# Kernel optimization log

Hardware: AMD Instinct MI355X
Metric: run time of the kernel (lower is better)

Reference implementation:

```python
import jax, jax.numpy as jnp
import numpy as np

DT = 1.0  # forward arg dt, fixed to its default
NOISE_KEY = 42

def _lin_init(k, fan_in, fan_out):
    kw, kb = jax.random.split(k)
    s = 1.0 / np.sqrt(fan_in)
    W = jax.random.uniform(kw, (fan_in, fan_out), minval=-s, maxval=s, dtype=jnp.float32)
    b = jax.random.uniform(kb, (fan_out,), minval=-s, maxval=s, dtype=jnp.float32)
    return W, b

def setup_inputs() -> dict:
    key = jax.random.key(0)
    ks = jax.random.split(key, 10)
    batch, d_model, hidden = 8, 512, 64
    in_dim = d_model + 2  # ctx + y + t
    W_f1, b_f1 = _lin_init(ks[0], in_dim, hidden)
    W_f2, b_f2 = _lin_init(ks[1], hidden, hidden)
    W_f3, b_f3 = _lin_init(ks[2], hidden, 1)
    W_g1, b_g1 = _lin_init(ks[3], in_dim, hidden)
    W_g2, b_g2 = _lin_init(ks[4], hidden, 1)
    W_mu, b_mu = _lin_init(ks[5], d_model, 1)
    W_sig, b_sig = _lin_init(ks[6], d_model, 1)
    h_t = jax.random.normal(ks[7], (batch, d_model), dtype=jnp.float32)
    # positive prices (log is taken); uniform in [0.5, 2.0)
    initial_price = jax.random.uniform(ks[8], (batch,), minval=0.5, maxval=2.0, dtype=jnp.float32)
    return dict(h_t=h_t, initial_price=initial_price,
                W_f1=W_f1, b_f1=b_f1, W_f2=W_f2, b_f2=b_f2, W_f3=W_f3, b_f3=b_f3,
                W_g1=W_g1, b_g1=b_g1, W_g2=W_g2, b_g2=b_g2,
                W_mu=W_mu, b_mu=b_mu, W_sig=W_sig, b_sig=b_sig,
                horizon=128, n_paths=4096)

def reference(h_t, initial_price, W_f1, b_f1, W_f2, b_f2, W_f3, b_f3,
              W_g1, b_g1, W_g2, b_g2, W_mu, b_mu, W_sig, b_sig,
              horizon, n_paths):
    batch, d = h_t.shape
    dtype = h_t.dtype
    mu = (h_t @ W_mu + b_mu)[:, 0]
    sigma = jax.nn.softplus(h_t @ W_sig + b_sig)[:, 0] + 1e-6
    # flatten (batch, n_paths) -> BN rows, broadcast context per path
    ctx = jnp.broadcast_to(h_t[:, None, :], (batch, n_paths, d)).reshape(batch * n_paths, d)
    y0 = jnp.broadcast_to(jnp.log(initial_price)[:, None], (batch, n_paths)).reshape(-1, 1)
    keys = jax.random.split(jax.random.key(NOISE_KEY), horizon)
    ts = jnp.arange(horizon, dtype=dtype) * jnp.asarray(DT, dtype)
    sqrt_dt = jnp.sqrt(jnp.asarray(DT, dtype))
    def step(y, xs):
        t, k = xs
        t_vec = jnp.broadcast_to(t, (y.shape[0], 1)).astype(dtype)
        inp = jnp.concatenate([ctx, y, t_vec], axis=-1)  # (BN, d+2)
        h1 = jax.nn.silu(inp @ W_f1 + b_f1)
        h2 = jax.nn.silu(h1 @ W_f2 + b_f2)
        f = h2 @ W_f3 + b_f3                              # drift (BN,1)
        g = jax.nn.softplus(jax.nn.silu(inp @ W_g1 + b_g1) @ W_g2 + b_g2) + 1e-6
        dW = jax.random.normal(k, y.shape, dtype) * sqrt_dt
        y_new = y + f * jnp.asarray(DT, dtype) + g * dW   # Euler-Maruyama (ito, diagonal)
        return y_new, y_new[:, 0]
    _, ys = jax.lax.scan(step, y0, (ts, keys))            # (horizon, BN)
    log_paths = jnp.clip(ys.T, -20.0, 20.0)               # (BN, horizon)
    paths = jnp.exp(log_paths).reshape(batch, n_paths, horizon)
    return paths, mu, sigma
```

## Files before the change

kernel.cpp:

```cpp
#include <hip/hip_runtime.h>
#include <stdint.h>

#define HOR 128
#define NPATH 4096
#define BATCH 8
#define DM 512
#define H 64
#define BN (BATCH*NPATH)

typedef __attribute__((ext_vector_type(8))) short s16x8;
typedef __attribute__((ext_vector_type(4))) float f32x4;

__device__ __forceinline__ uint32_t rotl32(uint32_t x, int r) {
  return (x << r) | (x >> (32 - r));
}

__device__ __forceinline__ void tf2x32(uint32_t k0, uint32_t k1,
                                       uint32_t& x0, uint32_t& x1) {
  uint32_t k2 = k0 ^ k1 ^ 0x1BD11BDAu;
  x0 += k0; x1 += k1;
#define TFR4(a,b,c,d) \
  x0 += x1; x1 = rotl32(x1,a); x1 ^= x0; \
  x0 += x1; x1 = rotl32(x1,b); x1 ^= x0; \
  x0 += x1; x1 = rotl32(x1,c); x1 ^= x0; \
  x0 += x1; x1 = rotl32(x1,d); x1 ^= x0;
  TFR4(13,15,26,6)  x0 += k1; x1 += k2 + 1u;
  TFR4(17,29,16,24) x0 += k2; x1 += k0 + 2u;
  TFR4(13,15,26,6)  x0 += k0; x1 += k1 + 3u;
  TFR4(17,29,16,24) x0 += k1; x1 += k2 + 4u;
  TFR4(13,15,26,6)  x0 += k2; x1 += k0 + 5u;
#undef TFR4
}

__device__ __forceinline__ float rcpf(float x) { return __builtin_amdgcn_rcpf(x); }
__device__ __forceinline__ float siluf(float x) {
  return x * rcpf(1.0f + __expf(-x));
}
__device__ __forceinline__ float softplusf(float x) {
  return fmaxf(x, 0.0f) + log1pf(__expf(-fabsf(x)));
}

__device__ __forceinline__ float bits_to_normal(uint32_t bits) {
  uint32_t fb = (bits >> 9) | 0x3F800000u;
  float f = __uint_as_float(fb) - 1.0f;
  float u = fmaf(f, 2.0f, -0.99999994f);
  u = fmaxf(u, -0.99999994f);
  float w = -log1pf(-u * u);
  float p;
  if (w < 5.0f) {
    w = w - 2.5f;
    p = 2.81022636e-08f;
    p = fmaf(p, w, 3.43273939e-07f);
    p = fmaf(p, w, -3.5233877e-06f);
    p = fmaf(p, w, -4.39150654e-06f);
    p = fmaf(p, w, 0.00021858087f);
    p = fmaf(p, w, -0.00125372503f);
    p = fmaf(p, w, -0.00417768164f);
    p = fmaf(p, w, 0.246640727f);
    p = fmaf(p, w, 1.50140941f);
  } else {
    w = sqrtf(w) - 3.0f;
    p = -0.000200214257f;
    p = fmaf(p, w, 0.000100950558f);
    p = fmaf(p, w, 0.00134934322f);
    p = fmaf(p, w, -0.00367342844f);
    p = fmaf(p, w, 0.00573950773f);
    p = fmaf(p, w, -0.0076224613f);
    p = fmaf(p, w, 0.00943887047f);
    p = fmaf(p, w, 1.00167406f);
    p = fmaf(p, w, 2.83297682f);
  }
  return 1.41421356237f * (p * u);
}

__device__ __forceinline__ uint32_t pack_hi16(uint32_t hi_src, uint32_t lo_src) {
  return __builtin_amdgcn_perm(hi_src, lo_src, 0x07060302u);
}

union FragU { uint32_t u[4]; s16x8 v; };

__device__ __forceinline__ void split3(const float (&x)[8],
                                       s16x8& fh, s16x8& fm, s16x8& fl) {
  FragU Hh, Mm, Ll;
  #pragma unroll
  for (int d = 0; d < 4; ++d) {
    float x0 = x[2*d], x1 = x[2*d+1];
    uint32_t a0 = __float_as_uint(x0), a1 = __float_as_uint(x1);
    float r10 = x0 - __uint_as_float(a0 & 0xFFFF0000u);
    float r11 = x1 - __uint_as_float(a1 & 0xFFFF0000u);
    uint32_t m0 = __float_as_uint(r10), m1 = __float_as_uint(r11);
    float r20 = r10 - __uint_as_float(m0 & 0xFFFF0000u);
    float r21 = r11 - __uint_as_float(m1 & 0xFFFF0000u);
    Hh.u[d] = pack_hi16(a1, a0);
    Mm.u[d] = pack_hi16(m1, m0);
    Ll.u[d] = pack_hi16(__float_as_uint(r21), __float_as_uint(r20));
  }
  fh = Hh.v; fm = Mm.v; fl = Ll.v;
}

#define MFMA16(A, B, C) __builtin_amdgcn_mfma_f32_16x16x32_bf16((A), (B), (C), 0, 0, 0)


__global__ void k_pre(const float* __restrict__ h_t,
                      const float* __restrict__ W_f1, const float* __restrict__ b_f1,
                      const float* __restrict__ W_g1, const float* __restrict__ b_g1,
                      const float* __restrict__ W_mu, const float* __restrict__ b_mu,
                      const float* __restrict__ W_sig, const float* __restrict__ b_sig,
                      float* __restrict__ out, float* __restrict__ ws) {
  int j = threadIdx.x;
  int b = blockIdx.x;
  if (b == 8) {
    uint32_t* keyA = (uint32_t*)ws + 1024;
    uint32_t* keyB = (uint32_t*)ws + 1152;
    for (int t = j; t < HOR; t += 64) {
      uint32_t x0 = 0u, x1 = (uint32_t)t;
      tf2x32(0u, 42u, x0, x1);
      keyA[t] = x0; keyB[t] = x1;
    }
    return;
  }
  const float* h = h_t + b * DM;
  float accF = b_f1[j], accG = b_g1[j];
  float pm = 0.0f, ps = 0.0f;
  #pragma unroll 4
  for (int d = 0; d < DM; ++d) {
    float hv = h[d];
    accF = fmaf(hv, W_f1[d * H + j], accF);
    accG = fmaf(hv, W_g1[d * H + j], accG);
  }
  ws[b * H + j] = accF;
  ws[512 + b * H + j] = accG;
  for (int d = j; d < DM; d += 64) {
    pm = fmaf(h[d], W_mu[d], pm);
    ps = fmaf(h[d], W_sig[d], ps);
  }
  #pragma unroll
  for (int off = 32; off > 0; off >>= 1) {
    pm += __shfl_down(pm, off);
    ps += __shfl_down(ps, off);
  }
  if (j == 0) {
    out[BN * HOR + b] = pm + b_mu[0];
    out[BN * HOR + 8 + b] = softplusf(ps + b_sig[0]) + 1e-6f;
  }
}

__global__ __launch_bounds__(256, 2)
void k_sde(const float* __restrict__ ip,
           const float* __restrict__ W_f1, const float* __restrict__ W_f2,
           const float* __restrict__ b_f2, const float* __restrict__ W_f3,
           const float* __restrict__ b_f3, const float* __restrict__ W_g1,
           const float* __restrict__ W_g2, const float* __restrict__ b_g2,
           float* __restrict__ out, const float* __restrict__ ws) {
  __shared__ __align__(16) float sW2[H * H];
  __shared__ __align__(16) float sF1y[H], sF1t[H], sBF[H];
  __shared__ __align__(16) float sGy[H], sGt[H], sBG[H], sG2[H];
  __shared__ __align__(16) float sF3[H], sBf2[H];
  __shared__ uint32_t sKA[HOR], sKB[HOR];

  const int tid  = threadIdx.x;
  const int rblk = blockIdx.x * 64;
  const int b    = rblk >> 12;

  #pragma unroll
  for (int m = 0; m < 16; ++m) sW2[tid + 256 * m] = W_f2[tid + 256 * m];
  if (tid < 64) {
    sF1y[tid] = W_f1[512 * H + tid];
    sF1t[tid] = W_f1[513 * H + tid];
    sGy[tid]  = W_g1[512 * H + tid];
    sGt[tid]  = W_g1[513 * H + tid];
    sF3[tid]  = W_f3[tid];
    sG2[tid]  = W_g2[tid];
    sBf2[tid] = b_f2[tid];
  } else if (tid < 128) {
    int i = tid - 64;
    sBF[i] = ws[b * H + i];
    sBG[i] = ws[512 + b * H + i];
  } else {
    const uint32_t* kws = (const uint32_t*)ws;
    int t = tid - 128;
    sKA[t] = kws[1024 + t];
    sKB[t] = kws[1152 + t];
  }
  __syncthreads();

  const int l  = tid & 63;
  const int wv = tid >> 6;
  const int rl = l & 15;
  const int h  = l >> 4;
  const int r  = rblk + wv * 16 + rl;

  s16x8 aw[4][2][3];
  #pragma unroll
  for (int mt = 0; mt < 4; ++mt) {
    #pragma unroll
    for (int s = 0; s < 2; ++s) {
      float xv[8];
      #pragma unroll
      for (int e = 0; e < 8; ++e)
        xv[e] = sW2[(32 * s + 8 * h + e) * H + 16 * mt + rl];
      split3(xv, aw[mt][s][0], aw[mt][s][1], aw[mt][s][2]);
    }
  }

  f32x4 f3v[4], bf2v[4];
  #pragma unroll
  for (int mt = 0; mt < 4; ++mt) {
    f3v[mt]  = *(const f32x4*)&sF3[16 * mt + 4 * h];
    bf2v[mt] = *(const f32x4*)&sBf2[16 * mt + 4 * h];
  }

  f32x4 wy[2][2], wt1[2][2], wb[2][2];
  #pragma unroll
  for (int s = 0; s < 2; ++s) {
    const int k0 = 32 * s + 8 * h;
    wy[s][0]  = *(const f32x4*)&sF1y[k0]; wy[s][1]  = *(const f32x4*)&sF1y[k0 + 4];
    wt1[s][0] = *(const f32x4*)&sF1t[k0]; wt1[s][1] = *(const f32x4*)&sF1t[k0 + 4];
    wb[s][0]  = *(const f32x4*)&sBF[k0];  wb[s][1]  = *(const f32x4*)&sBF[k0 + 4];
  }

  const float bf3 = b_f3[0];
  const float bg2 = b_g2[0];
  float y  = logf(ip[b]);
  float zz = 0.0f;
  float sb0 = 0.f, sb1 = 0.f, sb2 = 0.f, sb3 = 0.f;

  #pragma unroll 1
  for (int t = 0; t < HOR; ++t) {
    if ((t & 3) == 0) {
      const int tk = t + h;
      uint32_t x0 = 0u, x1 = (uint32_t)r;
      tf2x32(sKA[tk], sKB[tk], x0, x1);
      zz = bits_to_normal(x0 ^ x1);
    }
    const float z  = __shfl(zz, rl + 16 * (t & 3));
    const float tt = (float)t;

    f32x4 c[4];
    #pragma unroll
    for (int mt = 0; mt < 4; ++mt) c[mt] = bf2v[mt];

    s16x8 bh[2], bm[2], bl[2];
    #pragma unroll
    for (int s = 0; s < 2; ++s) {
      float hv[8];
      #pragma unroll
      for (int d2 = 0; d2 < 2; ++d2) {
        const f32x4 a_ = wy[s][d2], b_ = wt1[s][d2], cc = wb[s][d2];
        hv[4*d2+0] = siluf(fmaf(y, a_.x, fmaf(tt, b_.x, cc.x)));
        hv[4*d2+1] = siluf(fmaf(y, a_.y, fmaf(tt, b_.y, cc.y)));
        hv[4*d2+2] = siluf(fmaf(y, a_.z, fmaf(tt, b_.z, cc.z)));
        hv[4*d2+3] = siluf(fmaf(y, a_.w, fmaf(tt, b_.w, cc.w)));
      }
      split3(hv, bh[s], bm[s], bl[s]);
    }

    #pragma unroll
    for (int s = 0; s < 2; ++s) {
      #pragma unroll
      for (int mt = 0; mt < 4; ++mt) c[mt] = MFMA16(aw[mt][s][0], bh[s], c[mt]);
      #pragma unroll
      for (int mt = 0; mt < 4; ++mt) c[mt] = MFMA16(aw[mt][s][0], bm[s], c[mt]);
      #pragma unroll
      for (int mt = 0; mt < 4; ++mt) c[mt] = MFMA16(aw[mt][s][1], bh[s], c[mt]);
      #pragma unroll
      for (int mt = 0; mt < 4; ++mt) c[mt] = MFMA16(aw[mt][s][1], bm[s], c[mt]);
      #pragma unroll
      for (int mt = 0; mt < 4; ++mt) c[mt] = MFMA16(aw[mt][s][0], bl[s], c[mt]);
      #pragma unroll
      for (int mt = 0; mt < 4; ++mt) c[mt] = MFMA16(aw[mt][s][2], bh[s], c[mt]);
    }

    int kg = 8 * h;
    asm volatile("" : "+v"(kg));
    float ga = 0.0f;
    #pragma unroll
    for (int s = 0; s < 2; ++s) {
      const int k0 = kg + 32 * s;
      const f32x4 gy0 = *(const f32x4*)&sGy[k0], gy1 = *(const f32x4*)&sGy[k0 + 4];
      const f32x4 gt0 = *(const f32x4*)&sGt[k0], gt1 = *(const f32x4*)&sGt[k0 + 4];
      const f32x4 gb0 = *(const f32x4*)&sBG[k0], gb1 = *(const f32x4*)&sBG[k0 + 4];
      const f32x4 g20 = *(const f32x4*)&sG2[k0], g21 = *(const f32x4*)&sG2[k0 + 4];
      ga = fmaf(siluf(fmaf(y, gy0.x, fmaf(tt, gt0.x, gb0.x))), g20.x, ga);
      ga = fmaf(siluf(fmaf(y, gy0.y, fmaf(tt, gt0.y, gb0.y))), g20.y, ga);
      ga = fmaf(siluf(fmaf(y, gy0.z, fmaf(tt, gt0.z, gb0.z))), g20.z, ga);
      ga = fmaf(siluf(fmaf(y, gy0.w, fmaf(tt, gt0.w, gb0.w))), g20.w, ga);
      ga = fmaf(siluf(fmaf(y, gy1.x, fmaf(tt, gt1.x, gb1.x))), g21.x, ga);
      ga = fmaf(siluf(fmaf(y, gy1.y, fmaf(tt, gt1.y, gb1.y))), g21.y, ga);
      ga = fmaf(siluf(fmaf(y, gy1.z, fmaf(tt, gt1.z, gb1.z))), g21.z, ga);
      ga = fmaf(siluf(fmaf(y, gy1.w, fmaf(tt, gt1.w, gb1.w))), g21.w, ga);
    }
    ga += __shfl_xor(ga, 16);
    ga += __shfl_xor(ga, 32);
    const float gg = softplusf(bg2 + ga) + 1e-6f;

    float fa = 0.0f;
    #pragma unroll
    for (int mt = 0; mt < 4; ++mt) {
      fa = fmaf(siluf(c[mt].x), f3v[mt].x, fa);
      fa = fmaf(siluf(c[mt].y), f3v[mt].y, fa);
      fa = fmaf(siluf(c[mt].z), f3v[mt].z, fa);
      fa = fmaf(siluf(c[mt].w), f3v[mt].w, fa);
    }
    fa += __shfl_xor(fa, 16);
    fa += __shfl_xor(fa, 32);

    y = (y + (bf3 + fa)) + gg * z;
    const float yl = fminf(fmaxf(y, -20.0f), 20.0f);
    const float e  = __expf(yl);
    if (((t >> 2) & 3) == h) { sb0 = sb1; sb1 = sb2; sb2 = sb3; sb3 = e; }
    if ((t & 15) == 15) {
      f32x4 v; v.x = sb0; v.y = sb1; v.z = sb2; v.w = sb3;
      *(f32x4*)&out[(size_t)r * HOR + (t & ~15) + 4 * h] = v;
    }
  }
}

extern "C" void kernel_launch(void* const* d_in, const int* in_sizes, int n_in,
                              void* d_out, int out_size, void* d_ws, size_t ws_size,
                              hipStream_t stream) {
  const float* h_t   = (const float*)d_in[0];
  const float* ip    = (const float*)d_in[1];
  const float* W_f1  = (const float*)d_in[2];
  const float* b_f1  = (const float*)d_in[3];
  const float* W_f2  = (const float*)d_in[4];
  const float* b_f2  = (const float*)d_in[5];
  const float* W_f3  = (const float*)d_in[6];
  const float* b_f3  = (const float*)d_in[7];
  const float* W_g1  = (const float*)d_in[8];
  const float* b_g1  = (const float*)d_in[9];
  const float* W_g2  = (const float*)d_in[10];
  const float* b_g2  = (const float*)d_in[11];
  const float* W_mu  = (const float*)d_in[12];
  const float* b_mu  = (const float*)d_in[13];
  const float* W_sig = (const float*)d_in[14];
  const float* b_sig = (const float*)d_in[15];
  float* out = (float*)d_out;
  float* ws  = (float*)d_ws;

  hipLaunchKernelGGL(k_pre, dim3(9), dim3(64), 0, stream,
                     h_t, W_f1, b_f1, W_g1, b_g1, W_mu, b_mu, W_sig, b_sig, out, ws);
  hipLaunchKernelGGL(k_sde, dim3(BN / 64), dim3(256), 0, stream,
                     ip, W_f1, W_f2, b_f2, W_f3, b_f3, W_g1, W_g2, b_g2, out, ws);
}
```

Before: 528.9 us.

## Process two path groups per wave and pair SiLU reciprocals

Each wave now advances two independent 16-row groups of paths at once, so the serial recurrence gets two interleaved dependency chains. The MFMA weight fragments are reused across both groups and the block count is halved. SiLU is computed in pairs that share one reciprocal, softplus uses a fast log, and the reductions use split partial sums with a three-way shuffle. The cost is higher register pressure (launch bounds relaxed to 1 block), fewer blocks overall, and slightly different rounding.

```diff
diff --git a/kernel.cpp b/kernel.cpp
--- a/kernel.cpp
+++ b/kernel.cpp
@@ -36,8 +36,18 @@
 __device__ __forceinline__ float siluf(float x) {
   return x * rcpf(1.0f + __expf(-x));
 }
+__device__ __forceinline__ void silu2(float x0, float x1, float& o0, float& o1) {
+  const float e0 = __expf(-x0), e1 = __expf(-x1);
+  const float d0 = 1.0f + e0,   d1 = 1.0f + e1;
+  const float r  = rcpf(d0 * d1);
+  o0 = x0 * (r * d1);
+  o1 = x1 * (r * d0);
+}
 __device__ __forceinline__ float softplusf(float x) {
   return fmaxf(x, 0.0f) + log1pf(__expf(-fabsf(x)));
+}
+__device__ __forceinline__ float softplus_fast(float x) {
+  return fmaxf(x, 0.0f) + __logf(1.0f + __expf(-fabsf(x)));
 }
 
 __device__ __forceinline__ float bits_to_normal(uint32_t bits) {
@@ -145,7 +155,7 @@
   }
 }
 
-__global__ __launch_bounds__(256, 2)
+__global__ __launch_bounds__(256, 1)
 void k_sde(const float* __restrict__ ip,
            const float* __restrict__ W_f1, const float* __restrict__ W_f2,
            const float* __restrict__ b_f2, const float* __restrict__ W_f3,
@@ -159,7 +169,7 @@
   __shared__ uint32_t sKA[HOR], sKB[HOR];
 
   const int tid  = threadIdx.x;
-  const int rblk = blockIdx.x * 64;
+  const int rblk = blockIdx.x * 128;
   const int b    = rblk >> 12;
 
   #pragma unroll
@@ -188,7 +198,8 @@
   const int wv = tid >> 6;
   const int rl = l & 15;
   const int h  = l >> 4;
-  const int r  = rblk + wv * 16 + rl;
+  const int rA = rblk + wv * 32 + rl;
+  const int rB = rA + 16;
 
   s16x8 aw[4][2][3];
   #pragma unroll
@@ -221,97 +232,189 @@
 
   const float bf3 = b_f3[0];
   const float bg2 = b_g2[0];
-  float y  = logf(ip[b]);
-  float zz = 0.0f;
-  float sb0 = 0.f, sb1 = 0.f, sb2 = 0.f, sb3 = 0.f;
+  float yA = logf(ip[b]);
+  float yB = yA;
+  float zzA = 0.0f, zzB = 0.0f;
+  float sbA0 = 0.f, sbA1 = 0.f, sbA2 = 0.f, sbA3 = 0.f;
+  float sbB0 = 0.f, sbB1 = 0.f, sbB2 = 0.f, sbB3 = 0.f;
 
   #pragma unroll 1
   for (int t = 0; t < HOR; ++t) {
     if ((t & 3) == 0) {
       const int tk = t + h;
-      uint32_t x0 = 0u, x1 = (uint32_t)r;
+      uint32_t x0 = 0u, x1 = (uint32_t)rA;
       tf2x32(sKA[tk], sKB[tk], x0, x1);
-      zz = bits_to_normal(x0 ^ x1);
-    }
-    const float z  = __shfl(zz, rl + 16 * (t & 3));
+      zzA = bits_to_normal(x0 ^ x1);
+      uint32_t y0 = 0u, y1 = (uint32_t)rB;
+      tf2x32(sKA[tk], sKB[tk], y0, y1);
+      zzB = bits_to_normal(y0 ^ y1);
+    }
+    const float zA = __shfl(zzA, rl + 16 * (t & 3));
+    const float zB = __shfl(zzB, rl + 16 * (t & 3));
     const float tt = (float)t;
 
-    f32x4 c[4];
+    f32x4 cA[4], cB[4];
     #pragma unroll
-    for (int mt = 0; mt < 4; ++mt) c[mt] = bf2v[mt];
-
-    s16x8 bh[2], bm[2], bl[2];
+    for (int mt = 0; mt < 4; ++mt) { cA[mt] = bf2v[mt]; cB[mt] = bf2v[mt]; }
+
+    s16x8 bhA[2], bmA[2], blA[2], bhB[2], bmB[2], blB[2];
     #pragma unroll
     for (int s = 0; s < 2; ++s) {
-      float hv[8];
+      float pvA[8], pvB[8], hvA[8], hvB[8];
       #pragma unroll
       for (int d2 = 0; d2 < 2; ++d2) {
         const f32x4 a_ = wy[s][d2], b_ = wt1[s][d2], cc = wb[s][d2];
-        hv[4*d2+0] = siluf(fmaf(y, a_.x, fmaf(tt, b_.x, cc.x)));
-        hv[4*d2+1] = siluf(fmaf(y, a_.y, fmaf(tt, b_.y, cc.y)));
-        hv[4*d2+2] = siluf(fmaf(y, a_.z, fmaf(tt, b_.z, cc.z)));
-        hv[4*d2+3] = siluf(fmaf(y, a_.w, fmaf(tt, b_.w, cc.w)));
+        const float tb0 = fmaf(tt, b_.x, cc.x);
+        const float tb1 = fmaf(tt, b_.y, cc.y);
+        const float tb2 = fmaf(tt, b_.z, cc.z);
+        const float tb3 = fmaf(tt, b_.w, cc.w);
+        pvA[4*d2+0] = fmaf(yA, a_.x, tb0);  pvB[4*d2+0] = fmaf(yB, a_.x, tb0);
+        pvA[4*d2+1] = fmaf(yA, a_.y, tb1);  pvB[4*d2+1] = fmaf(yB, a_.y, tb1);
+        pvA[4*d2+2] = fmaf(yA, a_.z, tb2);  pvB[4*d2+2] = fmaf(yB, a_.z, tb2);
+        pvA[4*d2+3] = fmaf(yA, a_.w, tb3);  pvB[4*d2+3] = fmaf(yB, a_.w, tb3);
       }
-      split3(hv, bh[s], bm[s], bl[s]);
+      silu2(pvA[0], pvA[1], hvA[0], hvA[1]); silu2(pvB[0], pvB[1], hvB[0], hvB[1]);
+      silu2(pvA[2], pvA[3], hvA[2], hvA[3]); silu2(pvB[2], pvB[3], hvB[2], hvB[3]);
+      silu2(pvA[4], pvA[5], hvA[4], hvA[5]); silu2(pvB[4], pvB[5], hvB[4], hvB[5]);
+      silu2(pvA[6], pvA[7], hvA[6], hvA[7]); silu2(pvB[6], pvB[7], hvB[6], hvB[7]);
+      split3(hvA, bhA[s], bmA[s], blA[s]);
+      split3(hvB, bhB[s], bmB[s], blB[s]);
     }
 
     #pragma unroll
     for (int s = 0; s < 2; ++s) {
       #pragma unroll
-      for (int mt = 0; mt < 4; ++mt) c[mt] = MFMA16(aw[mt][s][0], bh[s], c[mt]);
-      #pragma unroll
-      for (int mt = 0; mt < 4; ++mt) c[mt] = MFMA16(aw[mt][s][0], bm[s], c[mt]);
-      #pragma unroll
-      for (int mt = 0; mt < 4; ++mt) c[mt] = MFMA16(aw[mt][s][1], bh[s], c[mt]);
-      #pragma unroll
-      for (int mt = 0; mt < 4; ++mt) c[mt] = MFMA16(aw[mt][s][1], bm[s], c[mt]);
-      #pragma unroll
-      for (int mt = 0; mt < 4; ++mt) c[mt] = MFMA16(aw[mt][s][0], bl[s], c[mt]);
-      #pragma unroll
-      for (int mt = 0; mt < 4; ++mt) c[mt] = MFMA16(aw[mt][s][2], bh[s], c[mt]);
+      for (int mt = 0; mt < 4; ++mt) { cA[mt] = MFMA16(aw[mt][s][0], bhA[s], cA[mt]);
+                                       cB[mt] = MFMA16(aw[mt][s][0], bhB[s], cB[mt]); }
+      #pragma unroll
+      for (int mt = 0; mt < 4; ++mt) { cA[mt] = MFMA16(aw[mt][s][0], bmA[s], cA[mt]);
+                                       cB[mt] = MFMA16(aw[mt][s][0], bmB[s], cB[mt]); }
+      #pragma unroll
+      for (int mt = 0; mt < 4; ++mt) { cA[mt] = MFMA16(aw[mt][s][1], bhA[s], cA[mt]);
+                                       cB[mt] = MFMA16(aw[mt][s][1], bhB[s], cB[mt]); }
+      #pragma unroll
+      for (int mt = 0; mt < 4; ++mt) { cA[mt] = MFMA16(aw[mt][s][1], bmA[s], cA[mt]);
+                                       cB[mt] = MFMA16(aw[mt][s][1], bmB[s], cB[mt]); }
+      #pragma unroll
+      for (int mt = 0; mt < 4; ++mt) { cA[mt] = MFMA16(aw[mt][s][0], blA[s], cA[mt]);
+                                       cB[mt] = MFMA16(aw[mt][s][0], blB[s], cB[mt]); }
+      #pragma unroll
+      for (int mt = 0; mt < 4; ++mt) { cA[mt] = MFMA16(aw[mt][s][2], bhA[s], cA[mt]);
+                                       cB[mt] = MFMA16(aw[mt][s][2], bhB[s], cB[mt]); }
     }
 
     int kg = 8 * h;
     asm volatile("" : "+v"(kg));
-    float ga = 0.0f;
-    #pragma unroll
-    for (int s = 0; s < 2; ++s) {
-      const int k0 = kg + 32 * s;
+    float gA0, gA1, gA2, gA3, gB0, gB1, gB2, gB3;
+    {
+      const int k0 = kg;
       const f32x4 gy0 = *(const f32x4*)&sGy[k0], gy1 = *(const f32x4*)&sGy[k0 + 4];
       const f32x4 gt0 = *(const f32x4*)&sGt[k0], gt1 = *(const f32x4*)&sGt[k0 + 4];
       const f32x4 gb0 = *(const f32x4*)&sBG[k0], gb1 = *(const f32x4*)&sBG[k0 + 4];
       const f32x4 g20 = *(const f32x4*)&sG2[k0], g21 = *(const f32x4*)&sG2[k0 + 4];
-      ga = fmaf(siluf(fmaf(y, gy0.x, fmaf(tt, gt0.x, gb0.x))), g20.x, ga);
-      ga = fmaf(siluf(fmaf(y, gy0.y, fmaf(tt, gt0.y, gb0.y))), g20.y, ga);
-      ga = fmaf(siluf(fmaf(y, gy0.z, fmaf(tt, gt0.z, gb0.z))), g20.z, ga);
-      ga = fmaf(siluf(fmaf(y, gy0.w, fmaf(tt, gt0.w, gb0.w))), g20.w, ga);
-      ga = fmaf(siluf(fmaf(y, gy1.x, fmaf(tt, gt1.x, gb1.x))), g21.x, ga);
-      ga = fmaf(siluf(fmaf(y, gy1.y, fmaf(tt, gt1.y, gb1.y))), g21.y, ga);
-      ga = fmaf(siluf(fmaf(y, gy1.z, fmaf(tt, gt1.z, gb1.z))), g21.z, ga);
-      ga = fmaf(siluf(fmaf(y, gy1.w, fmaf(tt, gt1.w, gb1.w))), g21.w, ga);
-    }
-    ga += __shfl_xor(ga, 16);
-    ga += __shfl_xor(ga, 32);
-    const float gg = softplusf(bg2 + ga) + 1e-6f;
-
-    float fa = 0.0f;
-    #pragma unroll
-    for (int mt = 0; mt < 4; ++mt) {
-      fa = fmaf(siluf(c[mt].x), f3v[mt].x, fa);
-      fa = fmaf(siluf(c[mt].y), f3v[mt].y, fa);
-      fa = fmaf(siluf(c[mt].z), f3v[mt].z, fa);
-      fa = fmaf(siluf(c[mt].w), f3v[mt].w, fa);
-    }
-    fa += __shfl_xor(fa, 16);
-    fa += __shfl_xor(fa, 32);
-
-    y = (y + (bf3 + fa)) + gg * z;
-    const float yl = fminf(fmaxf(y, -20.0f), 20.0f);
-    const float e  = __expf(yl);
-    if (((t >> 2) & 3) == h) { sb0 = sb1; sb1 = sb2; sb2 = sb3; sb3 = e; }
+      const float t0 = fmaf(tt, gt0.x, gb0.x), t1 = fmaf(tt, gt0.y, gb0.y);
+      const float t2 = fmaf(tt, gt0.z, gb0.z), t3 = fmaf(tt, gt0.w, gb0.w);
+      const float t4 = fmaf(tt, gt1.x, gb1.x), t5 = fmaf(tt, gt1.y, gb1.y);
+      const float t6 = fmaf(tt, gt1.z, gb1.z), t7 = fmaf(tt, gt1.w, gb1.w);
+      float sA0,sA1,sA2,sA3,sA4,sA5,sA6,sA7, sB0,sB1,sB2,sB3,sB4,sB5,sB6,sB7;
+      silu2(fmaf(yA, gy0.x, t0), fmaf(yA, gy0.y, t1), sA0, sA1);
+      silu2(fmaf(yB, gy0.x, t0), fmaf(yB, gy0.y, t1), sB0, sB1);
+      silu2(fmaf(yA, gy0.z, t2), fmaf(yA, gy0.w, t3), sA2, sA3);
+      silu2(fmaf(yB, gy0.z, t2), fmaf(yB, gy0.w, t3), sB2, sB3);
+      silu2(fmaf(yA, gy1.x, t4), fmaf(yA, gy1.y, t5), sA4, sA5);
+      silu2(fmaf(yB, gy1.x, t4), fmaf(yB, gy1.y, t5), sB4, sB5);
+      silu2(fmaf(yA, gy1.z, t6), fmaf(yA, gy1.w, t7), sA6, sA7);
+      silu2(fmaf(yB, gy1.z, t6), fmaf(yB, gy1.w, t7), sB6, sB7);
+      gA0 = sA0 * g20.x;  gA1 = sA1 * g20.y;  gA2 = sA2 * g20.z;  gA3 = sA3 * g20.w;
+      gB0 = sB0 * g20.x;  gB1 = sB1 * g20.y;  gB2 = sB2 * g20.z;  gB3 = sB3 * g20.w;
+      gA0 = fmaf(sA4, g21.x, gA0); gA1 = fmaf(sA5, g21.y, gA1);
+      gA2 = fmaf(sA6, g21.z, gA2); gA3 = fmaf(sA7, g21.w, gA3);
+      gB0 = fmaf(sB4, g21.x, gB0); gB1 = fmaf(sB5, g21.y, gB1);
+      gB2 = fmaf(sB6, g21.z, gB2); gB3 = fmaf(sB7, g21.w, gB3);
+    }
+    {
+      const int k0 = kg + 32;
+      const f32x4 gy0 = *(const f32x4*)&sGy[k0], gy1 = *(const f32x4*)&sGy[k0 + 4];
+      const f32x4 gt0 = *(const f32x4*)&sGt[k0], gt1 = *(const f32x4*)&sGt[k0 + 4];
+      const f32x4 gb0 = *(const f32x4*)&sBG[k0], gb1 = *(const f32x4*)&sBG[k0 + 4];
+      const f32x4 g20 = *(const f32x4*)&sG2[k0], g21 = *(const f32x4*)&sG2[k0 + 4];
+      const float t0 = fmaf(tt, gt0.x, gb0.x), t1 = fmaf(tt, gt0.y, gb0.y);
+      const float t2 = fmaf(tt, gt0.z, gb0.z), t3 = fmaf(tt, gt0.w, gb0.w);
+      const float t4 = fmaf(tt, gt1.x, gb1.x), t5 = fmaf(tt, gt1.y, gb1.y);
+      const float t6 = fmaf(tt, gt1.z, gb1.z), t7 = fmaf(tt, gt1.w, gb1.w);
+      float sA0,sA1,sA2,sA3,sA4,sA5,sA6,sA7, sB0,sB1,sB2,sB3,sB4,sB5,sB6,sB7;
+      silu2(fmaf(yA, gy0.x, t0), fmaf(yA, gy0.y, t1), sA0, sA1);
+      silu2(fmaf(yB, gy0.x, t0), fmaf(yB, gy0.y, t1), sB0, sB1);
+      silu2(fmaf(yA, gy0.z, t2), fmaf(yA, gy0.w, t3), sA2, sA3);
+      silu2(fmaf(yB, gy0.z, t2), fmaf(yB, gy0.w, t3), sB2, sB3);
+      silu2(fmaf(yA, gy1.x, t4), fmaf(yA, gy1.y, t5), sA4, sA5);
+      silu2(fmaf(yB, gy1.x, t4), fmaf(yB, gy1.y, t5), sB4, sB5);
+      silu2(fmaf(yA, gy1.z, t6), fmaf(yA, gy1.w, t7), sA6, sA7);
+      silu2(fmaf(yB, gy1.z, t6), fmaf(yB, gy1.w, t7), sB6, sB7);
+      gA0 = fmaf(sA0, g20.x, gA0); gA1 = fmaf(sA1, g20.y, gA1);
+      gA2 = fmaf(sA2, g20.z, gA2); gA3 = fmaf(sA3, g20.w, gA3);
+      gB0 = fmaf(sB0, g20.x, gB0); gB1 = fmaf(sB1, g20.y, gB1);
+      gB2 = fmaf(sB2, g20.z, gB2); gB3 = fmaf(sB3, g20.w, gB3);
+      gA0 = fmaf(sA4, g21.x, gA0); gA1 = fmaf(sA5, g21.y, gA1);
+      gA2 = fmaf(sA6, g21.z, gA2); gA3 = fmaf(sA7, g21.w, gA3);
+      gB0 = fmaf(sB4, g21.x, gB0); gB1 = fmaf(sB5, g21.y, gB1);
+      gB2 = fmaf(sB6, g21.z, gB2); gB3 = fmaf(sB7, g21.w, gB3);
+    }
+    const float gaA = (gA0 + gA1) + (gA2 + gA3);
+    const float gaB = (gB0 + gB1) + (gB2 + gB3);
+    const float gaAx = __shfl_xor(gaA, 16), gaAy = __shfl_xor(gaA, 32), gaAz = __shfl_xor(gaA, 48);
+    const float gaBx = __shfl_xor(gaB, 16), gaBy = __shfl_xor(gaB, 32), gaBz = __shfl_xor(gaB, 48);
+
+    float sA[16], sB[16];
+    silu2(cA[0].x, cA[0].y, sA[0],  sA[1]);  silu2(cB[0].x, cB[0].y, sB[0],  sB[1]);
+    silu2(cA[0].z, cA[0].w, sA[2],  sA[3]);  silu2(cB[0].z, cB[0].w, sB[2],  sB[3]);
+    silu2(cA[1].x, cA[1].y, sA[4],  sA[5]);  silu2(cB[1].x, cB[1].y, sB[4],  sB[5]);
+    silu2(cA[1].z, cA[1].w, sA[6],  sA[7]);  silu2(cB[1].z, cB[1].w, sB[6],  sB[7]);
+    silu2(cA[2].x, cA[2].y, sA[8],  sA[9]);  silu2(cB[2].x, cB[2].y, sB[8],  sB[9]);
+    silu2(cA[2].z, cA[2].w, sA[10], sA[11]); silu2(cB[2].z, cB[2].w, sB[10], sB[11]);
+    silu2(cA[3].x, cA[3].y, sA[12], sA[13]); silu2(cB[3].x, cB[3].y, sB[12], sB[13]);
+    silu2(cA[3].z, cA[3].w, sA[14], sA[15]); silu2(cB[3].z, cB[3].w, sB[14], sB[15]);
+    float fA0 = sA[0]  * f3v[0].x, fB0 = sB[0]  * f3v[0].x;
+    float fA1 = sA[4]  * f3v[1].x, fB1 = sB[4]  * f3v[1].x;
+    float fA2 = sA[8]  * f3v[2].x, fB2 = sB[8]  * f3v[2].x;
+    float fA3 = sA[12] * f3v[3].x, fB3 = sB[12] * f3v[3].x;
+    fA0 = fmaf(sA[1],  f3v[0].y, fA0); fB0 = fmaf(sB[1],  f3v[0].y, fB0);
+    fA1 = fmaf(sA[5],  f3v[1].y, fA1); fB1 = fmaf(sB[5],  f3v[1].y, fB1);
+    fA2 = fmaf(sA[9],  f3v[2].y, fA2); fB2 = fmaf(sB[9],  f3v[2].y, fB2);
+    fA3 = fmaf(sA[13], f3v[3].y, fA3); fB3 = fmaf(sB[13], f3v[3].y, fB3);
+    fA0 = fmaf(sA[2],  f3v[0].z, fA0); fB0 = fmaf(sB[2],  f3v[0].z, fB0);
+    fA1 = fmaf(sA[6],  f3v[1].z, fA1); fB1 = fmaf(sB[6],  f3v[1].z, fB1);
+    fA2 = fmaf(sA[10], f3v[2].z, fA2); fB2 = fmaf(sB[10], f3v[2].z, fB2);
+    fA3 = fmaf(sA[14], f3v[3].z, fA3); fB3 = fmaf(sB[14], f3v[3].z, fB3);
+    fA0 = fmaf(sA[3],  f3v[0].w, fA0); fB0 = fmaf(sB[3],  f3v[0].w, fB0);
+    fA1 = fmaf(sA[7],  f3v[1].w, fA1); fB1 = fmaf(sB[7],  f3v[1].w, fB1);
+    fA2 = fmaf(sA[11], f3v[2].w, fA2); fB2 = fmaf(sB[11], f3v[2].w, fB2);
+    fA3 = fmaf(sA[15], f3v[3].w, fA3); fB3 = fmaf(sB[15], f3v[3].w, fB3);
+    const float faA = (fA0 + fA1) + (fA2 + fA3);
+    const float faB = (fB0 + fB1) + (fB2 + fB3);
+    const float faAx = __shfl_xor(faA, 16), faAy = __shfl_xor(faA, 32), faAz = __shfl_xor(faA, 48);
+    const float faBx = __shfl_xor(faB, 16), faBy = __shfl_xor(faB, 32), faBz = __shfl_xor(faB, 48);
+
+    const float gaAT = (gaA + gaAx) + (gaAy + gaAz);
+    const float gaBT = (gaB + gaBx) + (gaBy + gaBz);
+    const float ggA  = softplus_fast(bg2 + gaAT) + 1e-6f;
+    const float ggB  = softplus_fast(bg2 + gaBT) + 1e-6f;
+    const float faAT = (faA + faAx) + (faAy + faAz);
+    const float faBT = (faB + faBx) + (faBy + faBz);
+
+    yA = (yA + (bf3 + faAT)) + ggA * zA;
+    yB = (yB + (bf3 + faBT)) + ggB * zB;
+    const float eA = __expf(fminf(fmaxf(yA, -20.0f), 20.0f));
+    const float eB = __expf(fminf(fmaxf(yB, -20.0f), 20.0f));
+    if (((t >> 2) & 3) == h) {
+      sbA0 = sbA1; sbA1 = sbA2; sbA2 = sbA3; sbA3 = eA;
+      sbB0 = sbB1; sbB1 = sbB2; sbB2 = sbB3; sbB3 = eB;
+    }
     if ((t & 15) == 15) {
-      f32x4 v; v.x = sb0; v.y = sb1; v.z = sb2; v.w = sb3;
-      *(f32x4*)&out[(size_t)r * HOR + (t & ~15) + 4 * h] = v;
+      f32x4 vA; vA.x = sbA0; vA.y = sbA1; vA.z = sbA2; vA.w = sbA3;
+      f32x4 vB; vB.x = sbB0; vB.y = sbB1; vB.z = sbB2; vB.w = sbB3;
+      *(f32x4*)&out[(size_t)rA * HOR + (t & ~15) + 4 * h] = vA;
+      *(f32x4*)&out[(size_t)rB * HOR + (t & ~15) + 4 * h] = vB;
     }
   }
 }
@@ -340,6 +443,6 @@
 
   hipLaunchKernelGGL(k_pre, dim3(9), dim3(64), 0, stream,
                      h_t, W_f1, b_f1, W_g1, b_g1, W_mu, b_mu, W_sig, b_sig, out, ws);
-  hipLaunchKernelGGL(k_sde, dim3(BN / 64), dim3(256), 0, stream,
+  hipLaunchKernelGGL(k_sde, dim3(BN / 128), dim3(256), 0, stream,
                      ip, W_f1, W_f2, b_f2, W_f3, b_f3, W_g1, W_g2, b_g2, out, ws);
 }
```

Measured after the change: 531.9 us. Within noise of the previous version (+0.6%).
